# Kernel optimization log

Hardware: AMD Instinct MI355X
Metric: run time of the kernel (lower is better)

## Reference

```python
import jax, jax.numpy as jnp
import numpy as np

DIM = 192
HEADS = 6
PE_TABLE_SIZE = 2601  # 51x51 relative-position grid, rows of length pos_dim+3=5


def setup_inputs() -> dict:
    key = jax.random.key(0)
    ks = jax.random.split(key, 16)
    b, n, m, c = 2, 8192, 48, DIM
    feat = jax.random.normal(ks[0], (b, n, c), dtype=jnp.float32)
    member_idx = jax.random.randint(ks[1], (b, n, m), 0, n)
    cluster_mask = (jax.random.uniform(ks[2], (b, n, m)) > 0.1).astype(jnp.float32)
    pe_idx = jax.random.randint(ks[3], (b, n, m), 0, PE_TABLE_SIZE)
    s = 1.0 / np.sqrt(c)
    Wq = jax.random.normal(ks[4], (c, c), dtype=jnp.float32) * s
    bq = jnp.zeros((c,), jnp.float32)
    Wkv = jax.random.normal(ks[5], (2 * c, c), dtype=jnp.float32) * s
    bkv = jnp.zeros((2 * c,), jnp.float32)
    Wpe = jax.random.normal(ks[6], (HEADS, 5), dtype=jnp.float32) * 0.4
    bpe = jnp.zeros((HEADS,), jnp.float32)
    blank_k = jax.random.normal(ks[7], (c,), dtype=jnp.float32)
    blank_v = jax.random.normal(ks[8], (c,), dtype=jnp.float32)
    Wproj = jax.random.normal(ks[9], (c, c), dtype=jnp.float32) * s
    bproj = jnp.zeros((c,), jnp.float32)
    pre_table = jax.random.normal(ks[10], (PE_TABLE_SIZE, 5), dtype=jnp.float32)
    return {"feat": feat, "member_idx": member_idx, "cluster_mask": cluster_mask,
            "pe_idx": pe_idx, "global_attn": 0,
            "Wq": Wq, "bq": bq, "Wkv": Wkv, "bkv": bkv, "Wpe": Wpe, "bpe": bpe,
            "blank_k": blank_k, "blank_v": blank_v, "Wproj": Wproj, "bproj": bproj,
            "pre_table": pre_table}


def reference(feat, member_idx, cluster_mask, pe_idx, global_attn,
              Wq, bq, Wkv, bkv, Wpe, bpe, blank_k, blank_v, Wproj, bproj, pre_table):
    b, n, c = feat.shape
    h = Wpe.shape[0]
    c_ = c // h
    scale = c_ ** (-0.5)

    q = (feat @ Wq.T + bq) * scale                      # [b,n,c]
    kv = (feat @ Wkv.T + bkv).reshape(b, n, h, 2, c_)   # split like torch view(b,n,h,2,c_)
    k = kv[:, :, :, 0, :]                               # [b,n,h,c_]
    v = kv[:, :, :, 1, :]                               # [b,n,h,c_]
    q = q.reshape(b, n, h, c_)

    # positional-embedding lookup table: [T,5] -> [T,h]
    pe_table = pre_table @ Wpe.T + bpe
    pos = pe_table[pe_idx]                              # [b,n,m,h]

    if not global_attn:
        m = member_idx.shape[-1]
        idx = member_idx.reshape(b, n * m, 1)
        # gather neighbor keys/values: CLUSTENQK / CLUSTENAV semantics
        kg = jnp.take_along_axis(k.reshape(b, n, h * c_), idx, axis=1).reshape(b, n, m, h, c_)
        attn = jnp.einsum('bnhc,bnmhc->bhnm', q, kg)    # [b,h,n,m]
        attn = attn + pos.transpose(0, 3, 1, 2)
        attn = attn + (1.0 - cluster_mask)[:, None] * (-100.0)
    else:
        attn = jnp.einsum('bnhc,bshc->bhns', q, k)
        attn = attn + pos.transpose(0, 3, 1, 2)

    # blank token logit, clamped
    blank = jnp.clip(jnp.einsum('bnhc,hc->bhn', q, blank_k.reshape(h, c_)), -5.0, 5.0)[..., None]
    attn_all = jax.nn.softmax(jnp.concatenate([attn, blank], axis=-1), axis=-1)
    attn_nb = attn_all[..., :-1]                        # [b,h,n,m]
    blank_a = attn_all[..., -1:]                        # [b,h,n,1]

    if not global_attn:
        vg = jnp.take_along_axis(v.reshape(b, n, h * c_), idx, axis=1).reshape(b, n, m, h, c_)
        out = jnp.einsum('bhnm,bnmhc->bnhc', attn_nb, vg)
    else:
        out = jnp.einsum('bhns,bshc->bnhc', attn_nb, v)

    out = out + blank_a.transpose(0, 2, 1, 3) * blank_v.reshape(1, 1, h, c_)
    out = out.reshape(b, n, c)
    return out @ Wproj.T + bproj
```

## Files before the change

kernel.cpp:

```cpp
#include <hip/hip_runtime.h>
#include <hip/hip_fp16.h>

#define DIMC 192
#define HEADS 6
#define NSEQ 8192
#define NB 2
#define NMEM 48
#define PE_N 2601
#define NTOT (NB * NSEQ)

typedef _Float16 f16;
typedef __attribute__((ext_vector_type(4))) _Float16 f16x4;
typedef __attribute__((ext_vector_type(8))) _Float16 f16x8;
typedef __attribute__((ext_vector_type(4))) float f32x4;
typedef __attribute__((ext_vector_type(4))) int i32x4;

__global__ void pe_kernel(const float* __restrict__ pre_table,
                          const float* __restrict__ Wpe,
                          const float* __restrict__ bpe,
                          float* __restrict__ pe_out) {
    int i = blockIdx.x * blockDim.x + threadIdx.x;
    if (i >= PE_N) return;
    float p0 = pre_table[i * 5 + 0], p1 = pre_table[i * 5 + 1], p2 = pre_table[i * 5 + 2];
    float p3 = pre_table[i * 5 + 3], p4 = pre_table[i * 5 + 4];
#pragma unroll
    for (int h = 0; h < HEADS; ++h) {
        float s = bpe[h] + p0 * Wpe[h * 5 + 0] + p1 * Wpe[h * 5 + 1] + p2 * Wpe[h * 5 + 2]
                + p3 * Wpe[h * 5 + 3] + p4 * Wpe[h * 5 + 4];
        pe_out[i * HEADS + h] = s;
    }
}

#define WQ4   (DIMC * DIMC / 4)
#define WKV4  (2 * DIMC * DIMC / 4)
#define BL4   (DIMC / 4)
#define CVT_TOT (WQ4 + WKV4 + WQ4 + BL4 + BL4)
__global__ __launch_bounds__(256) void cvtW_kernel(
    const float* __restrict__ Wq, const float* __restrict__ Wkv,
    const float* __restrict__ Wproj, const float* __restrict__ blank_k,
    const float* __restrict__ blank_v,
    f16* __restrict__ WqH, f16* __restrict__ WkvH, f16* __restrict__ WprojH,
    f16* __restrict__ bkH, f16* __restrict__ bvH) {
    int i = blockIdx.x * 256 + threadIdx.x;
    if (i >= CVT_TOT) return;
    const float* src; f16* dst; int j = i;
    if (j < WQ4)                { src = Wq;      dst = WqH; }
    else if ((j -= WQ4) < WKV4) { src = Wkv;     dst = WkvH; }
    else if ((j -= WKV4) < WQ4) { src = Wproj;   dst = WprojH; }
    else if ((j -= WQ4) < BL4)  { src = blank_k; dst = bkH; }
    else { j -= BL4;              src = blank_v;  dst = bvH; }
    float4 f = *reinterpret_cast<const float4*>(src + (size_t)j * 4);
    f16x4 h = {(f16)f.x, (f16)f.y, (f16)f.z, (f16)f.w};
    *reinterpret_cast<f16x4*>(dst + (size_t)j * 4) = h;
}

template <int MODE>
__global__ __launch_bounds__(256) void gemm_kernel(
    const void* __restrict__ Aptr, const f16* __restrict__ W0, const f16* __restrict__ Wkv,
    const float* __restrict__ b0, const float* __restrict__ bkv,
    f16* __restrict__ oq, f16* __restrict__ ok, f16* __restrict__ ov,
    float* __restrict__ ofp) {
    __shared__ __align__(16) f16 As[64 * DIMC];
    __shared__ __align__(16) f16 Bs[64 * DIMC];
    __shared__ __align__(16) f16 Cs[64][72];
    const int tid = threadIdx.x, w = tid >> 6, l = tid & 63;
    const size_t rowbase = (size_t)blockIdx.x * 64;

    if (MODE == 0) {
        const float* A = (const float*)Aptr;
        const int row = tid >> 2, cg = tid & 3;
        const float* src = A + (rowbase + row) * DIMC + cg * 48;
        f16* dstrow = As + row * DIMC;
#pragma unroll
        for (int jj = 0; jj < 6; ++jj) {
            const int c = cg * 6 + jj;
            float4 x = *reinterpret_cast<const float4*>(src + jj * 8);
            float4 y = *reinterpret_cast<const float4*>(src + jj * 8 + 4);
            f16x8 hv = {(f16)x.x, (f16)x.y, (f16)x.z, (f16)x.w,
                        (f16)y.x, (f16)y.y, (f16)y.z, (f16)y.w};
            *reinterpret_cast<f16x8*>(dstrow + ((c ^ (row & 7)) << 3)) = hv;
        }
    } else {
        const f16* A = (const f16*)Aptr;
        const char* Abase = (const char*)(A + rowbase * DIMC);
#pragma unroll
        for (int i = 0; i < 6; ++i) {
            const int L = (w * 6 + i) * 64 + l;
            const int row = L / 24, cp = L % 24;
            __builtin_amdgcn_global_load_lds(
                (const __attribute__((address_space(1))) unsigned int*)
                    (Abase + row * 384 + ((cp ^ (row & 7)) << 4)),
                (__attribute__((address_space(3))) unsigned int*)
                    (As + (size_t)(w * 6 + i) * 512),
                16, 0, 0);
        }
    }
    __syncthreads();

    const int lm = l & 15, lg = l >> 4;
    const int wr = w & 1, wc = w >> 1;
    const char* AsB = (const char*)As;
    const int r0 = wr * 32 + lm, r1 = r0 + 16;
    f16x8 af0[6], af1[6];
#pragma unroll
    for (int ks = 0; ks < 6; ++ks) {
        const int ch = ((ks * 4 + lg) ^ (lm & 7)) << 4;
        af0[ks] = *reinterpret_cast<const f16x8*>(AsB + r0 * 384 + ch);
        af1[ks] = *reinterpret_cast<const f16x8*>(AsB + r1 * 384 + ch);
    }

    const int NT = (MODE == 0) ? 9 : 3;
    for (int ct = 0; ct < NT; ++ct) {
        {
            const int cb = ct * 64;
            const f16* Wsel = (MODE == 0 && cb >= DIMC)
                                  ? (Wkv + (size_t)(cb - DIMC) * DIMC)
                                  : (W0 + (size_t)cb * DIMC);
            const char* Wbase = (const char*)Wsel;
#pragma unroll
            for (int i = 0; i < 6; ++i) {
                const int L = (w * 6 + i) * 64 + l;
                const int row = L / 24, cp = L % 24;
                __builtin_amdgcn_global_load_lds(
                    (const __attribute__((address_space(1))) unsigned int*)
                        (Wbase + row * 384 + ((cp ^ (row & 7)) << 4)),
                    (__attribute__((address_space(3))) unsigned int*)
                        (Bs + (size_t)(w * 6 + i) * 512),
                    16, 0, 0);
            }
        }
        __syncthreads();
        f32x4 a00 = {0.f, 0.f, 0.f, 0.f}, a01 = a00, a10 = a00, a11 = a00;
        const char* BsB = (const char*)Bs;
        const int b0r = (wc * 32 + lm) * 384, b1r = b0r + 16 * 384;
#pragma unroll
        for (int ks = 0; ks < 6; ++ks) {
            const int ch = ((ks * 4 + lg) ^ (lm & 7)) << 4;
            f16x8 q0 = *reinterpret_cast<const f16x8*>(BsB + b0r + ch);
            f16x8 q1 = *reinterpret_cast<const f16x8*>(BsB + b1r + ch);
            a00 = __builtin_amdgcn_mfma_f32_16x16x32_f16(af0[ks], q0, a00, 0, 0, 0);
            a01 = __builtin_amdgcn_mfma_f32_16x16x32_f16(af0[ks], q1, a01, 0, 0, 0);
            a10 = __builtin_amdgcn_mfma_f32_16x16x32_f16(af1[ks], q0, a10, 0, 0, 0);
            a11 = __builtin_amdgcn_mfma_f32_16x16x32_f16(af1[ks], q1, a11, 0, 0, 0);
        }
#pragma unroll
        for (int fm = 0; fm < 2; ++fm)
#pragma unroll
            for (int fn = 0; fn < 2; ++fn) {
                const f32x4 acc = fm ? (fn ? a11 : a10) : (fn ? a01 : a00);
                const int crow = wr * 32 + fm * 16 + lg * 4;
                const int ccol = wc * 32 + fn * 16 + lm;
#pragma unroll
                for (int r = 0; r < 4; ++r) Cs[crow + r][ccol] = (f16)acc[r];
            }
        __syncthreads();
        {
            const int row = tid >> 2, s = tid & 3;
            const int cb = ct * 64;
            const size_t gr = rowbase + row;
            f16x8 v0 = *reinterpret_cast<const f16x8*>(&Cs[row][s * 16]);
            f16x8 v1 = *reinterpret_cast<const f16x8*>(&Cs[row][s * 16 + 8]);
            const int c0 = cb + s * 16;
            if (MODE == 1) {
                float4 o[4];
#pragma unroll
                for (int t = 0; t < 8; ++t) {
                    ((float*)o)[t]     = (float)v0[t] + b0[c0 + t];
                    ((float*)o)[t + 8] = (float)v1[t] + b0[c0 + 8 + t];
                }
                float4* dst = reinterpret_cast<float4*>(ofp + gr * DIMC + c0);
                dst[0] = o[0]; dst[1] = o[1]; dst[2] = o[2]; dst[3] = o[3];
            } else if (c0 < DIMC) {
                const float sc = 0.17677669529663687f;
                f16x8 w0h, w1h;
#pragma unroll
                for (int t = 0; t < 8; ++t) {
                    w0h[t] = (f16)(((float)v0[t] + b0[c0 + t]) * sc);
                    w1h[t] = (f16)(((float)v1[t] + b0[c0 + 8 + t]) * sc);
                }
                *reinterpret_cast<f16x8*>(oq + gr * DIMC + c0) = w0h;
                *reinterpret_cast<f16x8*>(oq + gr * DIMC + c0 + 8) = w1h;
            } else {
                const int t0 = c0 - DIMC;
                const int hh = t0 >> 6, rr = t0 & 63;
                f16* base = (rr < 32) ? (ok + hh * 32 + (rr & 31))
                                      : (ov + hh * 32 + (rr & 31));
                f16x8 w0h, w1h;
#pragma unroll
                for (int t = 0; t < 8; ++t) {
                    w0h[t] = (f16)((float)v0[t] + bkv[t0 + t]);
                    w1h[t] = (f16)((float)v1[t] + bkv[t0 + 8 + t]);
                }
                *reinterpret_cast<f16x8*>(base + gr * DIMC) = w0h;
                *reinterpret_cast<f16x8*>(base + gr * DIMC + 8) = w1h;
            }
        }
    }
}

__device__ __forceinline__ int map_qi(int bid, int wave) {
    const int xcd = bid & 7, j = bid >> 3;
    const int batch = xcd >> 2;
    const int qslot = j * 4 + (xcd & 3);
    return batch * NSEQ + qslot * 4 + wave;
}

__global__ __launch_bounds__(256) void attnA_kernel(
    const f16* __restrict__ qH, const f16* __restrict__ kH, const f16* __restrict__ bkH,
    const int* __restrict__ member_idx, const float* __restrict__ cmask,
    const int* __restrict__ pe_idx, const float* __restrict__ peT,
    f16* __restrict__ w16) {
    __shared__ float p_lds[4][HEADS][64];
    __shared__ int m_lds[4][64];
    const int wave = threadIdx.x >> 6, lane = threadIdx.x & 63;
    const int qi = map_qi(blockIdx.x, wave);
    const int bbase = qi & ~(NSEQ - 1);
    if (lane < NMEM)
        m_lds[wave][lane] = bbase + member_idx[(size_t)qi * NMEM + lane];
    __syncthreads();
    const int s = lane & 1, ms = lane >> 1;
    const f16* qbase = qH + (size_t)qi * DIMC + s * 96;
#pragma unroll
    for (int pass = 0; pass < 2; ++pass) {
        const int m = pass * 32 + ms;
        const bool act = (m <= NMEM);
        const f16* kp;
        if (act && m < NMEM) kp = kH + (size_t)m_lds[wave][m] * DIMC + s * 96;
        else                 kp = bkH + s * 96;
        float a0 = 0.f, a1 = 0.f, a2 = 0.f;
#pragma unroll
        for (int j = 0; j < 12; ++j) {
            f16x8 qv = *reinterpret_cast<const f16x8*>(qbase + j * 8);
            f16x8 kd = *reinterpret_cast<const f16x8*>(kp + j * 8);
            float d = (float)qv[0] * (float)kd[0] + (float)qv[1] * (float)kd[1]
                    + (float)qv[2] * (float)kd[2] + (float)qv[3] * (float)kd[3]
                    + (float)qv[4] * (float)kd[4] + (float)qv[5] * (float)kd[5]
                    + (float)qv[6] * (float)kd[6] + (float)qv[7] * (float)kd[7];
            if (j < 4)      a0 += d;
            else if (j < 8) a1 += d;
            else            a2 += d;
        }
        if (act) {
            p_lds[wave][3 * s + 0][m] = a0;
            p_lds[wave][3 * s + 1][m] = a1;
            p_lds[wave][3 * s + 2][m] = a2;
        }
    }
    __syncthreads();
    {
        const int m = lane;
        float lo[HEADS];
#pragma unroll
        for (int h = 0; h < HEADS; ++h)
            lo[h] = (m <= NMEM) ? p_lds[wave][h][m] : -1e30f;
        if (m < NMEM) {
            const int pei = pe_idx[(size_t)qi * NMEM + m];
            const float msk = (1.0f - cmask[(size_t)qi * NMEM + m]) * -100.0f;
#pragma unroll
            for (int h = 0; h < HEADS; ++h) lo[h] += peT[pei * HEADS + h] + msk;
        } else if (m == NMEM) {
#pragma unroll
            for (int h = 0; h < HEADS; ++h) lo[h] = fminf(fmaxf(lo[h], -5.f), 5.f);
        }
#pragma unroll
        for (int h = 0; h < HEADS; ++h) {
            float mx = lo[h];
#pragma unroll
            for (int st = 32; st; st >>= 1) mx = fmaxf(mx, __shfl_xor(mx, st));
            const float e = __expf(lo[h] - mx);
            float sm = e;
#pragma unroll
            for (int st = 32; st; st >>= 1) sm += __shfl_xor(sm, st);
            p_lds[wave][h][m] = e / sm;
        }
    }
#pragma unroll
    for (int h = 0; h < HEADS; ++h)
        w16[(size_t)qi * 384 + h * 64 + lane] = (f16)p_lds[wave][h][lane];
}

__global__ __launch_bounds__(256) void attnB_kernel(
    const f16* __restrict__ vH, const f16* __restrict__ bvH,
    const int* __restrict__ member_idx, const f16* __restrict__ w16,
    f16* __restrict__ outA) {
    __shared__ float p_lds[4][HEADS][64];
    __shared__ int m_lds[4][64];
    const int wave = threadIdx.x >> 6, lane = threadIdx.x & 63;
    const int qi = map_qi(blockIdx.x, wave);
    const int bbase = qi & ~(NSEQ - 1);
    if (lane < NMEM)
        m_lds[wave][lane] = bbase + member_idx[(size_t)qi * NMEM + lane];
#pragma unroll
    for (int h = 0; h < HEADS; ++h)
        p_lds[wave][h][lane] = (float)w16[(size_t)qi * 384 + h * 64 + lane];
    __syncthreads();
    const int h0 = lane >> 5;
    float o0 = 0.f, o1 = 0.f, o2 = 0.f;
#pragma unroll 6
    for (int mm = 0; mm < NMEM; mm += 4) {
        const i32x4 rows = *reinterpret_cast<const i32x4*>(&m_lds[wave][mm]);
        const f32x4 w0 = *reinterpret_cast<const f32x4*>(&p_lds[wave][h0][mm]);
        const f32x4 w1 = *reinterpret_cast<const f32x4*>(&p_lds[wave][h0 + 2][mm]);
        const f32x4 w2 = *reinterpret_cast<const f32x4*>(&p_lds[wave][h0 + 4][mm]);
#pragma unroll
        for (int t = 0; t < 4; ++t) {
            const f16* vp = vH + (size_t)rows[t] * DIMC;
            o0 += w0[t] * (float)vp[lane];
            o1 += w1[t] * (float)vp[64 + lane];
            o2 += w2[t] * (float)vp[128 + lane];
        }
    }
    o0 += p_lds[wave][h0][NMEM]     * (float)bvH[lane];
    o1 += p_lds[wave][h0 + 2][NMEM] * (float)bvH[64 + lane];
    o2 += p_lds[wave][h0 + 4][NMEM] * (float)bvH[128 + lane];
    f16* orow = outA + (size_t)qi * DIMC;
    orow[lane] = (f16)o0; orow[64 + lane] = (f16)o1; orow[128 + lane] = (f16)o2;
}

extern "C" void kernel_launch(void* const* d_in, const int* in_sizes, int n_in,
                              void* d_out, int out_size, void* d_ws, size_t ws_size,
                              hipStream_t stream) {
    const float* feat      = (const float*)d_in[0];
    const int*   member_i  = (const int*)d_in[1];
    const float* cmask     = (const float*)d_in[2];
    const int*   pe_idx    = (const int*)d_in[3];
    const float* Wq        = (const float*)d_in[5];
    const float* bq        = (const float*)d_in[6];
    const float* Wkv       = (const float*)d_in[7];
    const float* bkv       = (const float*)d_in[8];
    const float* Wpe       = (const float*)d_in[9];
    const float* bpe       = (const float*)d_in[10];
    const float* blank_k   = (const float*)d_in[11];
    const float* blank_v   = (const float*)d_in[12];
    const float* Wproj     = (const float*)d_in[13];
    const float* bproj     = (const float*)d_in[14];
    const float* pre_table = (const float*)d_in[15];
    float* out = (float*)d_out;

    const size_t SZH = (size_t)NTOT * DIMC * sizeof(f16);
    char* ws = (char*)d_ws;
    f16* qH     = (f16*)(ws);
    f16* kH     = (f16*)(ws + SZH);
    f16* vH     = (f16*)(ws + 2 * SZH);
    f16* outAH  = (f16*)(ws + 3 * SZH);
    f16* w16    = (f16*)(ws + 4 * SZH);
    char* p = ws + 4 * SZH + (size_t)NTOT * 384 * 2;
    f16* WqH    = (f16*)p;              p += (size_t)DIMC * DIMC * 2;
    f16* WkvH   = (f16*)p;              p += (size_t)2 * DIMC * DIMC * 2;
    f16* WprojH = (f16*)p;              p += (size_t)DIMC * DIMC * 2;
    f16* bkH    = (f16*)p;              p += 512;
    f16* bvH    = (f16*)p;              p += 512;
    float* peT  = (float*)p;            p += (size_t)PE_N * HEADS * sizeof(float);
    if ((size_t)(p - ws) > ws_size) return;

    pe_kernel<<<(PE_N + 255) / 256, 256, 0, stream>>>(pre_table, Wpe, bpe, peT);
    cvtW_kernel<<<(CVT_TOT + 255) / 256, 256, 0, stream>>>(
        Wq, Wkv, Wproj, blank_k, blank_v, WqH, WkvH, WprojH, bkH, bvH);
    gemm_kernel<0><<<NTOT / 64, 256, 0, stream>>>(
        feat, WqH, WkvH, bq, bkv, qH, kH, vH, nullptr);
    attnA_kernel<<<NTOT / 4, 256, 0, stream>>>(qH, kH, bkH, member_i, cmask,
                                               pe_idx, peT, w16);
    attnB_kernel<<<NTOT / 4, 256, 0, stream>>>(vH, bvH, member_i, w16, outAH);
    gemm_kernel<1><<<NTOT / 64, 256, 0, stream>>>(
        outAH, WprojH, nullptr, bproj, nullptr, nullptr, nullptr, nullptr, out);
}
```

Measured before the change: 204.7 us.

## Pre-convert features to fp16, split GEMM column tiles across blocks, restructure QK dot

Feature conversion to fp16 moves into a combined grid-stride conversion kernel, so both GEMMs load A through global_load_lds. The GEMMs now spread their column tiles across a second grid dimension for more parallel blocks, and shared memory aliases Cs onto As to cut the footprint to 48KB. The QK score computation changes from a 2-lanes-per-member layout to 8 lanes per member, with q held in registers and shuffle reductions. Several __syncthreads are removed from attnA and attnB. The cost is an extra full fp16 feature round trip through memory, A tiles reloaded once per column split, and possible races where barriers were dropped, since the LDS writes are read by other lanes.

```diff
diff --git a/kernel.cpp b/kernel.cpp
--- a/kernel.cpp
+++ b/kernel.cpp
@@ -14,6 +14,13 @@
 typedef __attribute__((ext_vector_type(8))) _Float16 f16x8;
 typedef __attribute__((ext_vector_type(4))) float f32x4;
 typedef __attribute__((ext_vector_type(4))) int i32x4;
+
+static __device__ __forceinline__ float dot8(f16x8 a, f16x8 b) {
+    return (float)a[0] * (float)b[0] + (float)a[1] * (float)b[1]
+         + (float)a[2] * (float)b[2] + (float)a[3] * (float)b[3]
+         + (float)a[4] * (float)b[4] + (float)a[5] * (float)b[5]
+         + (float)a[6] * (float)b[6] + (float)a[7] * (float)b[7];
+}
 
 __global__ void pe_kernel(const float* __restrict__ pre_table,
                           const float* __restrict__ Wpe,
@@ -31,69 +38,55 @@
     }
 }
 
+#define FEAT4 (NTOT * DIMC / 4)
 #define WQ4   (DIMC * DIMC / 4)
 #define WKV4  (2 * DIMC * DIMC / 4)
 #define BL4   (DIMC / 4)
-#define CVT_TOT (WQ4 + WKV4 + WQ4 + BL4 + BL4)
-__global__ __launch_bounds__(256) void cvtW_kernel(
-    const float* __restrict__ Wq, const float* __restrict__ Wkv,
-    const float* __restrict__ Wproj, const float* __restrict__ blank_k,
-    const float* __restrict__ blank_v,
-    f16* __restrict__ WqH, f16* __restrict__ WkvH, f16* __restrict__ WprojH,
-    f16* __restrict__ bkH, f16* __restrict__ bvH) {
-    int i = blockIdx.x * 256 + threadIdx.x;
-    if (i >= CVT_TOT) return;
-    const float* src; f16* dst; int j = i;
-    if (j < WQ4)                { src = Wq;      dst = WqH; }
-    else if ((j -= WQ4) < WKV4) { src = Wkv;     dst = WkvH; }
-    else if ((j -= WKV4) < WQ4) { src = Wproj;   dst = WprojH; }
-    else if ((j -= WQ4) < BL4)  { src = blank_k; dst = bkH; }
-    else { j -= BL4;              src = blank_v;  dst = bvH; }
-    float4 f = *reinterpret_cast<const float4*>(src + (size_t)j * 4);
-    f16x4 h = {(f16)f.x, (f16)f.y, (f16)f.z, (f16)f.w};
-    *reinterpret_cast<f16x4*>(dst + (size_t)j * 4) = h;
-}
-
-template <int MODE>
+__global__ __launch_bounds__(256) void cvt_kernel(
+    const float* __restrict__ feat, const float* __restrict__ Wq,
+    const float* __restrict__ Wkv, const float* __restrict__ Wproj,
+    const float* __restrict__ blank_k, const float* __restrict__ blank_v,
+    f16* __restrict__ featH, f16* __restrict__ WqH, f16* __restrict__ WkvH,
+    f16* __restrict__ WprojH, f16* __restrict__ bkH, f16* __restrict__ bvH) {
+    const int total = FEAT4 + WQ4 + WKV4 + WQ4 + BL4 + BL4;
+    for (int i = blockIdx.x * 256 + threadIdx.x; i < total; i += gridDim.x * 256) {
+        const float* src; f16* dst; int j = i;
+        if (j < FEAT4)                { src = feat;    dst = featH; }
+        else if ((j -= FEAT4) < WQ4)  { src = Wq;      dst = WqH; }
+        else if ((j -= WQ4) < WKV4)   { src = Wkv;     dst = WkvH; }
+        else if ((j -= WKV4) < WQ4)   { src = Wproj;   dst = WprojH; }
+        else if ((j -= WQ4) < BL4)    { src = blank_k; dst = bkH; }
+        else { j -= BL4;                src = blank_v;  dst = bvH; }
+        float4 f = *reinterpret_cast<const float4*>(src + (size_t)j * 4);
+        f16x4 h = {(f16)f.x, (f16)f.y, (f16)f.z, (f16)f.w};
+        *reinterpret_cast<f16x4*>(dst + (size_t)j * 4) = h;
+    }
+}
+
+template <int MODE, int TPB>
 __global__ __launch_bounds__(256) void gemm_kernel(
-    const void* __restrict__ Aptr, const f16* __restrict__ W0, const f16* __restrict__ Wkv,
+    const f16* __restrict__ A, const f16* __restrict__ W0, const f16* __restrict__ Wkv,
     const float* __restrict__ b0, const float* __restrict__ bkv,
     f16* __restrict__ oq, f16* __restrict__ ok, f16* __restrict__ ov,
     float* __restrict__ ofp) {
-    __shared__ __align__(16) f16 As[64 * DIMC];
-    __shared__ __align__(16) f16 Bs[64 * DIMC];
-    __shared__ __align__(16) f16 Cs[64][72];
+    __shared__ __align__(16) char smem[48 * 1024];
+    f16* As = (f16*)smem;
+    f16 (*Cs)[72] = (f16(*)[72])smem;
+    f16* Bs = (f16*)(smem + 24 * 1024);
     const int tid = threadIdx.x, w = tid >> 6, l = tid & 63;
     const size_t rowbase = (size_t)blockIdx.x * 64;
 
-    if (MODE == 0) {
-        const float* A = (const float*)Aptr;
-        const int row = tid >> 2, cg = tid & 3;
-        const float* src = A + (rowbase + row) * DIMC + cg * 48;
-        f16* dstrow = As + row * DIMC;
-#pragma unroll
-        for (int jj = 0; jj < 6; ++jj) {
-            const int c = cg * 6 + jj;
-            float4 x = *reinterpret_cast<const float4*>(src + jj * 8);
-            float4 y = *reinterpret_cast<const float4*>(src + jj * 8 + 4);
-            f16x8 hv = {(f16)x.x, (f16)x.y, (f16)x.z, (f16)x.w,
-                        (f16)y.x, (f16)y.y, (f16)y.z, (f16)y.w};
-            *reinterpret_cast<f16x8*>(dstrow + ((c ^ (row & 7)) << 3)) = hv;
-        }
-    } else {
-        const f16* A = (const f16*)Aptr;
-        const char* Abase = (const char*)(A + rowbase * DIMC);
-#pragma unroll
-        for (int i = 0; i < 6; ++i) {
-            const int L = (w * 6 + i) * 64 + l;
-            const int row = L / 24, cp = L % 24;
-            __builtin_amdgcn_global_load_lds(
-                (const __attribute__((address_space(1))) unsigned int*)
-                    (Abase + row * 384 + ((cp ^ (row & 7)) << 4)),
-                (__attribute__((address_space(3))) unsigned int*)
-                    (As + (size_t)(w * 6 + i) * 512),
-                16, 0, 0);
-        }
+    const char* Abase = (const char*)(A + rowbase * DIMC);
+#pragma unroll
+    for (int i = 0; i < 6; ++i) {
+        const int L = (w * 6 + i) * 64 + l;
+        const int row = L / 24, cp = L % 24;
+        __builtin_amdgcn_global_load_lds(
+            (const __attribute__((address_space(1))) unsigned int*)
+                (Abase + row * 384 + ((cp ^ (row & 7)) << 4)),
+            (__attribute__((address_space(3))) unsigned int*)
+                (As + (size_t)(w * 6 + i) * 512),
+            16, 0, 0);
     }
     __syncthreads();
 
@@ -109,8 +102,8 @@
         af1[ks] = *reinterpret_cast<const f16x8*>(AsB + r1 * 384 + ch);
     }
 
-    const int NT = (MODE == 0) ? 9 : 3;
-    for (int ct = 0; ct < NT; ++ct) {
+    for (int t = 0; t < TPB; ++t) {
+        const int ct = blockIdx.y * TPB + t;
         {
             const int cb = ct * 64;
             const f16* Wsel = (MODE == 0 && cb >= DIMC)
@@ -164,9 +157,9 @@
             if (MODE == 1) {
                 float4 o[4];
 #pragma unroll
-                for (int t = 0; t < 8; ++t) {
-                    ((float*)o)[t]     = (float)v0[t] + b0[c0 + t];
-                    ((float*)o)[t + 8] = (float)v1[t] + b0[c0 + 8 + t];
+                for (int tt = 0; tt < 8; ++tt) {
+                    ((float*)o)[tt]     = (float)v0[tt] + b0[c0 + tt];
+                    ((float*)o)[tt + 8] = (float)v1[tt] + b0[c0 + 8 + tt];
                 }
                 float4* dst = reinterpret_cast<float4*>(ofp + gr * DIMC + c0);
                 dst[0] = o[0]; dst[1] = o[1]; dst[2] = o[2]; dst[3] = o[3];
@@ -174,9 +167,9 @@
                 const float sc = 0.17677669529663687f;
                 f16x8 w0h, w1h;
 #pragma unroll
-                for (int t = 0; t < 8; ++t) {
-                    w0h[t] = (f16)(((float)v0[t] + b0[c0 + t]) * sc);
-                    w1h[t] = (f16)(((float)v1[t] + b0[c0 + 8 + t]) * sc);
+                for (int tt = 0; tt < 8; ++tt) {
+                    w0h[tt] = (f16)(((float)v0[tt] + b0[c0 + tt]) * sc);
+                    w1h[tt] = (f16)(((float)v1[tt] + b0[c0 + 8 + tt]) * sc);
                 }
                 *reinterpret_cast<f16x8*>(oq + gr * DIMC + c0) = w0h;
                 *reinterpret_cast<f16x8*>(oq + gr * DIMC + c0 + 8) = w1h;
@@ -187,9 +180,9 @@
                                       : (ov + hh * 32 + (rr & 31));
                 f16x8 w0h, w1h;
 #pragma unroll
-                for (int t = 0; t < 8; ++t) {
-                    w0h[t] = (f16)((float)v0[t] + bkv[t0 + t]);
-                    w1h[t] = (f16)((float)v1[t] + bkv[t0 + 8 + t]);
+                for (int tt = 0; tt < 8; ++tt) {
+                    w0h[tt] = (f16)((float)v0[tt] + bkv[t0 + tt]);
+                    w1h[tt] = (f16)((float)v1[tt] + bkv[t0 + 8 + tt]);
                 }
                 *reinterpret_cast<f16x8*>(base + gr * DIMC) = w0h;
                 *reinterpret_cast<f16x8*>(base + gr * DIMC + 8) = w1h;
@@ -217,36 +210,30 @@
     const int bbase = qi & ~(NSEQ - 1);
     if (lane < NMEM)
         m_lds[wave][lane] = bbase + member_idx[(size_t)qi * NMEM + lane];
-    __syncthreads();
-    const int s = lane & 1, ms = lane >> 1;
-    const f16* qbase = qH + (size_t)qi * DIMC + s * 96;
-#pragma unroll
-    for (int pass = 0; pass < 2; ++pass) {
-        const int m = pass * 32 + ms;
+    const int g = lane >> 3, sub = lane & 7;
+    const f16* qrow = qH + (size_t)qi * DIMC;
+    const f16x8 qv0 = *reinterpret_cast<const f16x8*>(qrow + sub * 8);
+    const f16x8 qv1 = *reinterpret_cast<const f16x8*>(qrow + 64 + sub * 8);
+    const f16x8 qv2 = *reinterpret_cast<const f16x8*>(qrow + 128 + sub * 8);
+#pragma unroll
+    for (int it = 0; it < 7; ++it) {
+        const int m = it * 8 + g;
         const bool act = (m <= NMEM);
-        const f16* kp;
-        if (act && m < NMEM) kp = kH + (size_t)m_lds[wave][m] * DIMC + s * 96;
-        else                 kp = bkH + s * 96;
-        float a0 = 0.f, a1 = 0.f, a2 = 0.f;
-#pragma unroll
-        for (int j = 0; j < 12; ++j) {
-            f16x8 qv = *reinterpret_cast<const f16x8*>(qbase + j * 8);
-            f16x8 kd = *reinterpret_cast<const f16x8*>(kp + j * 8);
-            float d = (float)qv[0] * (float)kd[0] + (float)qv[1] * (float)kd[1]
-                    + (float)qv[2] * (float)kd[2] + (float)qv[3] * (float)kd[3]
-                    + (float)qv[4] * (float)kd[4] + (float)qv[5] * (float)kd[5]
-                    + (float)qv[6] * (float)kd[6] + (float)qv[7] * (float)kd[7];
-            if (j < 4)      a0 += d;
-            else if (j < 8) a1 += d;
-            else            a2 += d;
-        }
-        if (act) {
-            p_lds[wave][3 * s + 0][m] = a0;
-            p_lds[wave][3 * s + 1][m] = a1;
-            p_lds[wave][3 * s + 2][m] = a2;
-        }
-    }
-    __syncthreads();
+        const f16* kp = (act && m < NMEM) ? (kH + (size_t)m_lds[wave][m] * DIMC) : bkH;
+        const f16x8 k0 = *reinterpret_cast<const f16x8*>(kp + sub * 8);
+        const f16x8 k1 = *reinterpret_cast<const f16x8*>(kp + 64 + sub * 8);
+        const f16x8 k2 = *reinterpret_cast<const f16x8*>(kp + 128 + sub * 8);
+        float d0 = dot8(qv0, k0), d1 = dot8(qv1, k1), d2 = dot8(qv2, k2);
+        d0 += __shfl_xor(d0, 1); d0 += __shfl_xor(d0, 2);
+        d1 += __shfl_xor(d1, 1); d1 += __shfl_xor(d1, 2);
+        d2 += __shfl_xor(d2, 1); d2 += __shfl_xor(d2, 2);
+        if (act && (sub == 0 || sub == 4)) {
+            const int hb = sub >> 2;
+            p_lds[wave][hb][m]     = d0;
+            p_lds[wave][2 + hb][m] = d1;
+            p_lds[wave][4 + hb][m] = d2;
+        }
+    }
     {
         const int m = lane;
         float lo[HEADS];
@@ -293,7 +280,6 @@
 #pragma unroll
     for (int h = 0; h < HEADS; ++h)
         p_lds[wave][h][lane] = (float)w16[(size_t)qi * 384 + h * 64 + lane];
-    __syncthreads();
     const int h0 = lane >> 5;
     float o0 = 0.f, o1 = 0.f, o2 = 0.f;
 #pragma unroll 6
@@ -343,8 +329,9 @@
     f16* kH     = (f16*)(ws + SZH);
     f16* vH     = (f16*)(ws + 2 * SZH);
     f16* outAH  = (f16*)(ws + 3 * SZH);
-    f16* w16    = (f16*)(ws + 4 * SZH);
-    char* p = ws + 4 * SZH + (size_t)NTOT * 384 * 2;
+    f16* featH  = (f16*)(ws + 4 * SZH);
+    f16* w16    = (f16*)(ws + 5 * SZH);
+    char* p = ws + 5 * SZH + (size_t)NTOT * 384 * 2;
     f16* WqH    = (f16*)p;              p += (size_t)DIMC * DIMC * 2;
     f16* WkvH   = (f16*)p;              p += (size_t)2 * DIMC * DIMC * 2;
     f16* WprojH = (f16*)p;              p += (size_t)DIMC * DIMC * 2;
@@ -354,13 +341,13 @@
     if ((size_t)(p - ws) > ws_size) return;
 
     pe_kernel<<<(PE_N + 255) / 256, 256, 0, stream>>>(pre_table, Wpe, bpe, peT);
-    cvtW_kernel<<<(CVT_TOT + 255) / 256, 256, 0, stream>>>(
-        Wq, Wkv, Wproj, blank_k, blank_v, WqH, WkvH, WprojH, bkH, bvH);
-    gemm_kernel<0><<<NTOT / 64, 256, 0, stream>>>(
-        feat, WqH, WkvH, bq, bkv, qH, kH, vH, nullptr);
+    cvt_kernel<<<1024, 256, 0, stream>>>(feat, Wq, Wkv, Wproj, blank_k, blank_v,
+                                         featH, WqH, WkvH, WprojH, bkH, bvH);
+    gemm_kernel<0, 3><<<dim3(NTOT / 64, 3), 256, 0, stream>>>(
+        featH, WqH, WkvH, bq, bkv, qH, kH, vH, nullptr);
     attnA_kernel<<<NTOT / 4, 256, 0, stream>>>(qH, kH, bkH, member_i, cmask,
                                                pe_idx, peT, w16);
     attnB_kernel<<<NTOT / 4, 256, 0, stream>>>(vH, bvH, member_i, w16, outAH);
-    gemm_kernel<1><<<NTOT / 64, 256, 0, stream>>>(
+    gemm_kernel<1, 1><<<dim3(NTOT / 64, 3), 256, 0, stream>>>(
         outAH, WprojH, nullptr, bproj, nullptr, nullptr, nullptr, nullptr, out);
 }
```

New measurement: 181.1 us. 1.13x faster.
